# Performance work log

Hardware: AMD Instinct MI355X
Metric: run time of the kernel (lower is better)

The kernel has to match this reference:

```python
import jax, jax.numpy as jnp
import numpy as np

EPS = 1e-5
LAMB = 1.0
N_VARS = 40000
N_EDGES = 200000
N_CONF = 100000
FEAT = 128
DOM = 4
T_MAX = 3


def setup_inputs() -> dict:
    key = jax.random.key(0)
    ks = jax.random.split(key, 16)
    # initial node states: torch.rand then row-normalized (F.normalize dim=1)
    s = jax.random.uniform(ks[0], (N_VARS, FEAT), dtype=jnp.float32)
    state0 = s / jnp.maximum(jnp.linalg.norm(s, axis=1, keepdims=True), 1e-12)
    def lin(k, fan_in, shape):
        return jax.random.normal(k, shape, dtype=jnp.float32) / np.sqrt(fan_in)
    inp = {
        'state0': state0,
        'W1': lin(ks[1], 2 * FEAT, (2 * FEAT, FEAT)),
        'b1': jnp.zeros((FEAT,), jnp.float32),
        'W2': lin(ks[2], FEAT, (FEAT, FEAT)),
        'b2': jnp.zeros((FEAT,), jnp.float32),
        'ln_g': jnp.ones((FEAT,), jnp.float32),
        'ln_b': jnp.zeros((FEAT,), jnp.float32),
        'bn_g': jnp.ones((FEAT,), jnp.float32),
        'bn_b': jnp.zeros((FEAT,), jnp.float32),
        'Wd': lin(ks[3], FEAT, (FEAT, DOM)),
        'bd': jnp.zeros((DOM,), jnp.float32),
        # positive relation/confidence matrices so -log(...) is finite
        'relation': jax.random.uniform(ks[4], (DOM, DOM), jnp.float32, 0.1, 1.0),
        'confidence_mat': jax.random.uniform(ks[5], (DOM, DOM), jnp.float32, 0.1, 1.0),
        # positive degrees (divisor)
        'degrees': jax.random.uniform(ks[6], (N_VARS,), jnp.float32, 1.0, 33.0),
        'idx_left': jax.random.randint(ks[7], (N_EDGES,), 0, N_VARS, jnp.int32),
        'idx_right': jax.random.randint(ks[8], (N_EDGES,), 0, N_VARS, jnp.int32),
        'idx_left_pos': jax.random.randint(ks[9], (N_CONF,), 0, N_VARS, jnp.int32),
        'idx_right_pos': jax.random.randint(ks[10], (N_CONF,), 0, N_VARS, jnp.int32),
        'iterations': T_MAX,
    }
    return inp


def reference(state0, W1, b1, W2, b2, ln_g, ln_b, bn_g, bn_b, Wd, bd,
              relation, confidence_mat, degrees,
              idx_left, idx_right, idx_left_pos, idx_right_pos, iterations):
    N, F = state0.shape
    E = idx_left.shape[0]
    degs = degrees[:, None]

    def mlp(x):  # Linear-ReLU-Linear-ReLU-LayerNorm
        h = jax.nn.relu(x @ W1 + b1)
        h = jax.nn.relu(h @ W2 + b2)
        mu = jnp.mean(h, axis=-1, keepdims=True)
        var = jnp.var(h, axis=-1, keepdims=True)  # biased, like torch LayerNorm
        return ln_g * (h - mu) * jax.lax.rsqrt(var + EPS) + ln_b

    state = state0
    logits_list = []
    for _ in range(iterations):
        xl = state[idx_left]          # [E, F] gather
        xr = state[idx_right]
        # mpnn(in_right=xl, in_left=xr): in_lr = cat(xr, xl); in_rl = cat(xl, xr)
        msg = jnp.concatenate([jnp.concatenate([xr, xl], axis=1),
                               jnp.concatenate([xl, xr], axis=1)], axis=0)  # [2E, 2F]
        h = mlp(msg)
        agg = (jnp.zeros((N, F), state.dtype)
               .at[idx_left].add(h[:E])
               .at[idx_right].add(h[E:]))  # scatter-add messages
        rec = agg / degs
        # BatchNorm1d, training mode (batch stats over nodes)
        mu = jnp.mean(rec, axis=0)
        var = jnp.var(rec, axis=0)
        state = bn_g * (rec - mu) * jax.lax.rsqrt(var + EPS) + bn_b
        logits_list.append(state @ Wd + bd)

    phi = jax.nn.softmax(jnp.stack(logits_list, axis=1), axis=2)  # [N, T, D]
    T, D = phi.shape[1], phi.shape[2]
    all_phi = phi.reshape(N, T * D)

    def pair_loss(mat, il, ir, denom):
        pl = all_phi[il].reshape(-1, D)   # [E*T, D]
        pr = all_phi[ir].reshape(-1, D)
        s = jnp.sum((pl @ mat) * pr, axis=1)
        return jnp.sum(-jnp.log(s)) / denom

    n_conflicts = jnp.float32(E)
    n_confidence = jnp.float32(idx_left_pos.shape[0])
    loss = (pair_loss(relation, idx_left, idx_right, n_conflicts)
            + LAMB * pair_loss(confidence_mat, idx_left_pos, idx_right_pos, 10.0 * n_confidence))

    assignment = jnp.argmax(phi, axis=2).astype(jnp.int32)  # [N, T]
    valid = relation[assignment[idx_left], assignment[idx_right]]  # [E, T]
    edge_conflicts = 1.0 - valid
    n_conf = jnp.sum(edge_conflicts[:, -1])
    conflict_ratio = n_conf / n_conflicts
    return (loss, conflict_ratio, phi, edge_conflicts, assignment[:, -1], n_conf)
```

## Files before the change

kernel.cpp:

```cpp
#include <hip/hip_runtime.h>
#include <math.h>

#define N_VARS 40000
#define FEAT 128
#define N_EDGES 200000
#define N_MSG (2*N_EDGES)
#define N_CONFP 100000
#define T_ITERS 3
#define EPSF 1e-5f

#define NB_CONF 782
#define NB_LOSS 3517
#define NB_STAT 157
#define OUT_TOTAL 1120003
#define NCONF_SLOT 1120002

typedef short short8 __attribute__((ext_vector_type(8)));
typedef float floatx4 __attribute__((ext_vector_type(4)));
typedef unsigned short ushort4v __attribute__((ext_vector_type(4)));

__device__ __forceinline__ float scrub0(float x){
  unsigned u = __float_as_uint(x);
  return ((u & 0x7F800000u) == 0x7F800000u) ? 0.f : x;
}
__device__ __forceinline__ unsigned short f2bf_rne(float x){
  unsigned u = __float_as_uint(x);
  u += 0x7FFFu + ((u >> 16) & 1u);
  return (unsigned short)(u >> 16);
}
__device__ __forceinline__ float bf2f(unsigned short h){
  return __uint_as_float(((unsigned)h) << 16);
}
__device__ __forceinline__ unsigned cvtpk(float lo, float hi){
  unsigned r;
  asm("v_cvt_pk_bf16_f32 %0, %1, %2" : "=v"(r) : "v"(lo), "v"(hi));
  return r;
}

__global__ __launch_bounds__(256) void k_zero_int(int* __restrict__ p, int n){
  int i = blockIdx.x*256 + threadIdx.x;
  if (i < n) p[i] = 0;
}

__global__ __launch_bounds__(256) void k_hist(const int* __restrict__ idxL,
    const int* __restrict__ idxR, int* __restrict__ cnt){
  int m = blockIdx.x*256 + threadIdx.x;
  if (m < N_MSG){
    int t = (m < N_EDGES) ? idxL[m] : idxR[m - N_EDGES];
    atomicAdd(&cnt[t], 1);
  }
}
__global__ __launch_bounds__(256) void k_scan1(const int* __restrict__ cnt,
    int* __restrict__ pos, int* __restrict__ blk_tot){
  const int tid = threadIdx.x;
  const int idx = blockIdx.x*256 + tid;
  int v = (idx < N_VARS) ? cnt[idx] : 0;
  __shared__ int sh[256];
  sh[tid] = v;
  __syncthreads();
#pragma unroll
  for (int o = 1; o < 256; o <<= 1){
    int add = (tid >= o) ? sh[tid - o] : 0;
    __syncthreads();
    sh[tid] += add;
    __syncthreads();
  }
  if (idx < N_VARS) pos[idx] = sh[tid] - v;
  if (tid == 255) blk_tot[blockIdx.x] = sh[255];
}
__global__ __launch_bounds__(256) void k_scan2(const int* __restrict__ blk_tot,
    int* __restrict__ blk_off){
  const int tid = threadIdx.x;
  int v = (tid < NB_STAT) ? blk_tot[tid] : 0;
  __shared__ int sh[256];
  sh[tid] = v;
  __syncthreads();
#pragma unroll
  for (int o = 1; o < 256; o <<= 1){
    int add = (tid >= o) ? sh[tid - o] : 0;
    __syncthreads();
    sh[tid] += add;
    __syncthreads();
  }
  if (tid < NB_STAT) blk_off[tid] = sh[tid] - v;
}
__global__ __launch_bounds__(256) void k_scan3(int* __restrict__ pos,
    const int* __restrict__ blk_off){
  const int idx = blockIdx.x*256 + threadIdx.x;
  if (idx < N_VARS) pos[idx] += blk_off[blockIdx.x];
}
__global__ __launch_bounds__(256) void k_fill(const int* __restrict__ idxL,
    const int* __restrict__ idxR, int* __restrict__ pos,
    int* __restrict__ morder, int* __restrict__ nodeof){
  int m = blockIdx.x*256 + threadIdx.x;
  if (m < N_MSG){
    int t = (m < N_EDGES) ? idxL[m] : idxR[m - N_EDGES];
    int slot = atomicAdd(&pos[t], 1);
    morder[slot] = m;
    nodeof[slot] = t;
  }
}

__global__ __launch_bounds__(256) void k_prep(const float* __restrict__ W2,
                                              unsigned short* __restrict__ W2pack){
  int gid = blockIdx.x*256 + threadIdx.x;
  int lane = gid & 63;
  int ks = (gid >> 6) & 3;
  int ntg = gid >> 8;
  int kbase = ks*32 + (lane >> 4)*8;
  int n = ntg*16 + (lane & 15);
#pragma unroll
  for (int j = 0; j < 8; ++j)
    W2pack[gid*8 + j] = f2bf_rne(W2[(kbase + j)*FEAT + n]);
}
__global__ __launch_bounds__(256) void k_prep_w1(const float* __restrict__ W1,
                                                 unsigned short* __restrict__ W1pack){
  int gid = blockIdx.x*256 + threadIdx.x;
  int lane = gid & 63;
  int ks = (gid >> 6) & 3;
  int ntg = gid >> 8;
  int kbase = ks*32 + (lane >> 4)*8;
  int n = ntg*16 + (lane & 15);
#pragma unroll
  for (int j = 0; j < 8; ++j){
    int k = kbase + j;
    float v = (n < 128) ? W1[k*FEAT + n] : W1[(128 + k)*FEAT + (n - 128)];
    W1pack[gid*8 + j] = f2bf_rne(v);
  }
}

#define X_STRIDE 136
__global__ __launch_bounds__(256) void k_pq(const float* __restrict__ xf,
                                            const unsigned short* __restrict__ xb,
                                            int src_f32,
                                            const unsigned short* __restrict__ W1pack,
                                            const float* __restrict__ b1v,
                                            unsigned short* __restrict__ PQb,
                                            float* __restrict__ red,
                                            float4* __restrict__ recz){
  __shared__ __align__(16) unsigned short Xbf[32*X_STRIDE];
  const int tid = threadIdx.x;
  const int row0 = blockIdx.x * 32;
  if (blockIdx.x == 0) red[tid] = 0.f;
  {
    const int zid = blockIdx.x*256 + tid;
#pragma unroll
    for (int i = 0; i < 4; ++i)
      recz[zid + i*320000] = make_float4(0.f,0.f,0.f,0.f);
  }
  if (src_f32){
    const int c4 = (tid & 31)*4, g8 = tid >> 5;
#pragma unroll
    for (int r = 0; r < 4; ++r){
      int row = g8*4 + r;
      const float4 v = *(const float4*)&xf[(row0 + row)*FEAT + c4];
      uint2 uu;
      uu.x = cvtpk(v.x, v.y);
      uu.y = cvtpk(v.z, v.w);
      *(uint2*)&Xbf[row*X_STRIDE + c4] = uu;
    }
  } else {
    const int c8 = (tid & 15)*8, g16 = tid >> 4;
#pragma unroll
    for (int r = 0; r < 2; ++r){
      int row = r*16 + g16;
      *(short8*)&Xbf[row*X_STRIDE + c8] = *(const short8*)&xb[(row0 + row)*FEAT + c8];
    }
  }
  __syncthreads();
  const int w = tid >> 6, lane = tid & 63;
  const int quad = lane >> 4, mcol = lane & 15;
  float bi0 = 0.f, bi1 = 0.f, bi2 = 0.f, bi3 = 0.f;
  if (w >= 2){
    int nb = (w - 2)*64 + mcol;
    bi0 = b1v[nb]; bi1 = b1v[nb + 16]; bi2 = b1v[nb + 32]; bi3 = b1v[nb + 48];
  }
#pragma unroll
  for (int mt = 0; mt < 2; ++mt){
    floatx4 a0 = {bi0,bi0,bi0,bi0};
    floatx4 a1 = {bi1,bi1,bi1,bi1};
    floatx4 a2 = {bi2,bi2,bi2,bi2};
    floatx4 a3 = {bi3,bi3,bi3,bi3};
#pragma unroll
    for (int ks = 0; ks < 4; ++ks){
      short8 a = *(const short8*)&Xbf[(mt*16 + mcol)*X_STRIDE + ks*32 + quad*8];
      const unsigned short* bp = W1pack + ((w*16 + ks)*64 + lane)*8;
      short8 b0 = *(const short8*)(bp);
      short8 b1 = *(const short8*)(bp + 2048);
      short8 b2 = *(const short8*)(bp + 4096);
      short8 b3 = *(const short8*)(bp + 6144);
      a0 = __builtin_amdgcn_mfma_f32_16x16x32_bf16(a, b0, a0, 0, 0, 0);
      a1 = __builtin_amdgcn_mfma_f32_16x16x32_bf16(a, b1, a1, 0, 0, 0);
      a2 = __builtin_amdgcn_mfma_f32_16x16x32_bf16(a, b2, a2, 0, 0, 0);
      a3 = __builtin_amdgcn_mfma_f32_16x16x32_bf16(a, b3, a3, 0, 0, 0);
    }
#pragma unroll
    for (int reg = 0; reg < 4; ++reg){
      unsigned u01 = cvtpk(a0[reg], a1[reg]);
      unsigned u23 = cvtpk(a2[reg], a3[reg]);
      size_t base = (size_t)(row0 + mt*16 + quad*4 + reg)*(2*FEAT) + w*64 + mcol;
      PQb[base]      = (unsigned short)u01;
      PQb[base + 16] = (unsigned short)(u01 >> 16);
      PQb[base + 32] = (unsigned short)u23;
      PQb[base + 48] = (unsigned short)(u23 >> 16);
    }
  }
}

#define U_STRIDE 136
#define ZT_STRIDE 68

__global__ __launch_bounds__(256) void k_msgagg(const unsigned short* __restrict__ PQb,
    const unsigned short* __restrict__ W2pack,
    const float* __restrict__ b2v, const float* __restrict__ ln_g, const float* __restrict__ ln_b,
    const int* __restrict__ idxL, const int* __restrict__ idxR,
    const int* __restrict__ morder, const int* __restrict__ nodeof,
    const float* __restrict__ degrees,
    float* __restrict__ rec){
  __shared__ __align__(16) unsigned short Ubf[64*U_STRIDE];
  __shared__ int sTa[64], sTb[64];
  __shared__ float sDinv[64];
  __shared__ int sEdge[2];
  const int tid = threadIdx.x;
  const int s0 = blockIdx.x * 64;
  if (tid < 64){
    int m = morder[s0 + tid];
    int e = (m < N_EDGES) ? m : (m - N_EDGES);
    int l = idxL[e], r = idxR[e];
    int ta = (m < N_EDGES) ? l : r;
    sTa[tid] = ta;
    sTb[tid] = (m < N_EDGES) ? r : l;
    sDinv[tid] = 1.f / degrees[ta];
  } else if (tid == 64){
    sEdge[0] = (s0 == 0) ? -1 : nodeof[s0 - 1];
  } else if (tid == 65){
    sEdge[1] = (s0 + 64 >= N_MSG) ? -1 : nodeof[s0 + 64];
  }
  __syncthreads();
  {
    const int c8 = (tid & 15)*8, g16 = tid >> 4;
    short8 pb[4], qb[4];
#pragma unroll
    for (int r = 0; r < 4; ++r){
      int row = r*16 + g16;
      pb[r] = *(const short8*)&PQb[sTb[row]*(2*FEAT) + c8];
      qb[r] = *(const short8*)&PQb[sTa[row]*(2*FEAT) + FEAT + c8];
    }
#pragma unroll
    for (int r = 0; r < 4; ++r){
      int row = r*16 + g16;
      float f[8];
#pragma unroll
      for (int j = 0; j < 8; ++j)
        f[j] = fmaxf(bf2f((unsigned short)pb[r][j]) + bf2f((unsigned short)qb[r][j]), 0.f);
      uint4 uu;
      uu.x = cvtpk(f[0], f[1]);
      uu.y = cvtpk(f[2], f[3]);
      uu.z = cvtpk(f[4], f[5]);
      uu.w = cvtpk(f[6], f[7]);
      *(uint4*)&Ubf[row*U_STRIDE + c8] = uu;
    }
  }
  __syncthreads();
  const int w = tid >> 6, lane = tid & 63;
  const int quad = lane >> 4, mcol = lane & 15;
  const int rbase = w*16;
  floatx4 acc[8];
#pragma unroll
  for (int nt = 0; nt < 8; ++nt){
    float b = b2v[nt*16 + mcol];
    acc[nt] = (floatx4){b, b, b, b};
  }
#pragma unroll
  for (int ks = 0; ks < 4; ++ks){
    short8 a = *(const short8*)&Ubf[(rbase + mcol)*U_STRIDE + ks*32 + quad*8];
#pragma unroll
    for (int nt = 0; nt < 8; ++nt){
      short8 b = *(const short8*)(W2pack + ((nt*4 + ks)*64 + lane)*8);
      acc[nt] = __builtin_amdgcn_mfma_f32_16x16x32_bf16(a, b, acc[nt], 0, 0, 0);
    }
  }
  float z[8][4];
#pragma unroll
  for (int nt = 0; nt < 8; ++nt){
#pragma unroll
    for (int reg = 0; reg < 4; ++reg) z[nt][reg] = fmaxf(acc[nt][reg], 0.f);
  }
  float ps[4], pq[4];
#pragma unroll
  for (int reg = 0; reg < 4; ++reg){
    ps[reg] = 0.f; pq[reg] = 0.f;
#pragma unroll
    for (int nt = 0; nt < 8; ++nt){
      ps[reg] += z[nt][reg];
      pq[reg] += z[nt][reg]*z[nt][reg];
    }
  }
#pragma unroll
  for (int o = 1; o < 16; o <<= 1){
#pragma unroll
    for (int reg = 0; reg < 4; ++reg){
      ps[reg] += __shfl_xor(ps[reg], o);
      pq[reg] += __shfl_xor(pq[reg], o);
    }
  }
  float lgv[8], lbv[8];
#pragma unroll
  for (int nt = 0; nt < 8; ++nt){
    lgv[nt] = ln_g[nt*16 + mcol];
    lbv[nt] = ln_b[nt*16 + mcol];
  }
  unsigned obp[4][4];
#pragma unroll
  for (int reg = 0; reg < 4; ++reg){
    float mu = ps[reg] * (1.f/FEAT);
    float var = fmaxf(pq[reg] * (1.f/FEAT) - mu*mu, 0.f);
    float rv = rsqrtf(var + EPSF);
#pragma unroll
    for (int np = 0; np < 4; ++np){
      float o0 = scrub0(lgv[2*np  ]*(z[2*np  ][reg] - mu)*rv + lbv[2*np  ]);
      float o1 = scrub0(lgv[2*np+1]*(z[2*np+1][reg] - mu)*rv + lbv[2*np+1]);
      obp[reg][np] = cvtpk(o0, o1);
    }
  }
  __syncthreads();
#pragma unroll
  for (int reg = 0; reg < 4; ++reg){
    int row = rbase + quad*4 + reg;
#pragma unroll
    for (int np = 0; np < 4; ++np){
      unsigned u = obp[reg][np];
      Ubf[(2*np*16 + mcol)*ZT_STRIDE + row]       = (unsigned short)u;
      Ubf[((2*np+1)*16 + mcol)*ZT_STRIDE + row]   = (unsigned short)(u >> 16);
    }
  }
  __syncthreads();
  {
    const int col = tid & 127, h = tid >> 7;
    const int rbeg = h*32;
    ushort4v rv4[8];
#pragma unroll
    for (int k = 0; k < 8; ++k)
      rv4[k] = *(const ushort4v*)&Ubf[col*ZT_STRIDE + rbeg + k*4];
    float accv = 0.f;
    int cur = sTa[rbeg];
    bool part = (rbeg == 0) ? (sEdge[0] == cur) : (sTa[rbeg-1] == cur);
#pragma unroll
    for (int i = 0; i < 32; ++i){
      accv += bf2f((unsigned short)rv4[i >> 2][i & 3]);
      const int r = rbeg + i;
      int nxt = (r < 63) ? sTa[r + 1] : -2;
      const bool lastr = (i == 31);
      if (lastr | (nxt != cur)){
        bool tail = lastr && ((r == 63) ? (sEdge[1] == cur) : (nxt == cur));
        float v = accv * sDinv[r];
        float* dst = &rec[(size_t)cur*FEAT + col];
        if (part | tail) atomicAdd(dst, v);
        else *dst = v;
        accv = 0.f;
        cur = nxt;
        part = false;
      }
    }
  }
}

__global__ __launch_bounds__(256) void k_edge(const unsigned short* __restrict__ PQb,
    const unsigned short* __restrict__ W2pack,
    const float* __restrict__ b2v, const float* __restrict__ ln_g, const float* __restrict__ ln_b,
    const int* __restrict__ idxL, const int* __restrict__ idxR,
    float* __restrict__ agg){
  __shared__ __align__(16) unsigned short Ubf[32*U_STRIDE];
  __shared__ float sS[64], sQ[64];
  __shared__ int sTa[32], sTb[32];
  const int tid = threadIdx.x;
  const int m0 = blockIdx.x * 32;
  if (tid < 32){
    int m = m0 + tid;
    int e = (m < N_EDGES) ? m : (m - N_EDGES);
    int l = idxL[e], r = idxR[e];
    sTa[tid] = (m < N_EDGES) ? l : r;
    sTb[tid] = (m < N_EDGES) ? r : l;
  }
  __syncthreads();
  {
    const int c8 = (tid & 15)*8, g16 = tid >> 4;
#pragma unroll
    for (int r = 0; r < 2; ++r){
      int row = r*16 + g16;
      short8 pb = *(const short8*)&PQb[sTb[row]*(2*FEAT) + c8];
      short8 qb = *(const short8*)&PQb[sTa[row]*(2*FEAT) + FEAT + c8];
      float f[8];
#pragma unroll
      for (int j = 0; j < 8; ++j)
        f[j] = fmaxf(bf2f((unsigned short)pb[j]) + bf2f((unsigned short)qb[j]), 0.f);
      uint4 uu;
      uu.x = cvtpk(f[0], f[1]);
      uu.y = cvtpk(f[2], f[3]);
      uu.z = cvtpk(f[4], f[5]);
      uu.w = cvtpk(f[6], f[7]);
      *(uint4*)&Ubf[row*U_STRIDE + c8] = uu;
    }
  }
  __syncthreads();
  const int w = tid >> 6, lane = tid & 63;
  const int mt = w & 1, nhalf = w >> 1;
  const int quad = lane >> 4, mcol = lane & 15;
  float bb0 = b2v[nhalf*64 + 0*16 + mcol];
  float bb1 = b2v[nhalf*64 + 1*16 + mcol];
  float bb2 = b2v[nhalf*64 + 2*16 + mcol];
  float bb3 = b2v[nhalf*64 + 3*16 + mcol];
  floatx4 acc0 = {bb0,bb0,bb0,bb0};
  floatx4 acc1 = {bb1,bb1,bb1,bb1};
  floatx4 acc2 = {bb2,bb2,bb2,bb2};
  floatx4 acc3 = {bb3,bb3,bb3,bb3};
#pragma unroll
  for (int ks = 0; ks < 4; ++ks){
    short8 a = *(const short8*)&Ubf[(mt*16 + mcol)*U_STRIDE + ks*32 + quad*8];
    const unsigned short* bp = W2pack + ((nhalf*4*256) + ks*64 + lane)*8;
    short8 bq0 = *(const short8*)(bp);
    short8 bq1 = *(const short8*)(bp + 2048);
    short8 bq2 = *(const short8*)(bp + 4096);
    short8 bq3 = *(const short8*)(bp + 6144);
    acc0 = __builtin_amdgcn_mfma_f32_16x16x32_bf16(a, bq0, acc0, 0, 0, 0);
    acc1 = __builtin_amdgcn_mfma_f32_16x16x32_bf16(a, bq1, acc1, 0, 0, 0);
    acc2 = __builtin_amdgcn_mfma_f32_16x16x32_bf16(a, bq2, acc2, 0, 0, 0);
    acc3 = __builtin_amdgcn_mfma_f32_16x16x32_bf16(a, bq3, acc3, 0, 0, 0);
  }
  float z[4][4];
#pragma unroll
  for (int nt = 0; nt < 4; ++nt){
    floatx4 a4 = (nt == 0) ? acc0 : (nt == 1) ? acc1 : (nt == 2) ? acc2 : acc3;
#pragma unroll
    for (int reg = 0; reg < 4; ++reg) z[nt][reg] = fmaxf(a4[reg], 0.f);
  }
  float ps[4], pq[4];
#pragma unroll
  for (int reg = 0; reg < 4; ++reg){
    ps[reg] = z[0][reg] + z[1][reg] + z[2][reg] + z[3][reg];
    pq[reg] = z[0][reg]*z[0][reg] + z[1][reg]*z[1][reg] + z[2][reg]*z[2][reg] + z[3][reg]*z[3][reg];
  }
#pragma unroll
  for (int o = 1; o < 16; o <<= 1){
#pragma unroll
    for (int reg = 0; reg < 4; ++reg){
      ps[reg] += __shfl_xor(ps[reg], o);
      pq[reg] += __shfl_xor(pq[reg], o);
    }
  }
  if (mcol == 0){
#pragma unroll
    for (int reg = 0; reg < 4; ++reg){
      int row = mt*16 + quad*4 + reg;
      sS[nhalf*32 + row] = ps[reg];
      sQ[nhalf*32 + row] = pq[reg];
    }
  }
  __syncthreads();
  int colv[4]; float lgv[4], lbv[4];
#pragma unroll
  for (int nt = 0; nt < 4; ++nt){
    colv[nt] = nhalf*64 + nt*16 + mcol;
    lgv[nt] = ln_g[colv[nt]];
    lbv[nt] = ln_b[colv[nt]];
  }
#pragma unroll
  for (int reg = 0; reg < 4; ++reg){
    int row = mt*16 + quad*4 + reg;
    float s = sS[row] + sS[32 + row];
    float q = sQ[row] + sQ[32 + row];
    float mu = s * (1.f/FEAT);
    float var = fmaxf(q * (1.f/FEAT) - mu*mu, 0.f);
    float rv = rsqrtf(var + EPSF);
    int a = sTa[row];
#pragma unroll
    for (int nt = 0; nt < 4; ++nt){
      float o = scrub0(lgv[nt]*(z[nt][reg] - mu)*rv + lbv[nt]);
      atomicAdd(&agg[a*FEAT + colv[nt]], o);
    }
  }
}

__global__ __launch_bounds__(256) void k_stats(const float* __restrict__ src,
    const float* __restrict__ degrees, int divide, float* __restrict__ red){
  const int tid = threadIdx.x;
  const int j = tid & 127, half_sel = tid >> 7;
  const int n0 = blockIdx.x * 256;
  float s1 = 0.f, s2 = 0.f;
  for (int i = half_sel; i < 256; i += 2){
    int n = n0 + i;
    if (n < N_VARS){
      float v = src[n*FEAT + j];
      if (divide) v /= degrees[n];
      s1 += v;
      s2 += v*v;
    }
  }
  __shared__ float sh1[256], sh2[256];
  sh1[tid] = s1; sh2[tid] = s2;
  __syncthreads();
  if (half_sel == 0){
    atomicAdd(&red[j],       sh1[tid] + sh1[tid+128]);
    atomicAdd(&red[128 + j], sh2[tid] + sh2[tid+128]);
  }
}

__global__ __launch_bounds__(256) void k_bn(const float* __restrict__ src,
    const float* __restrict__ degrees, int divide, const float* __restrict__ red,
    const float* __restrict__ bn_g, const float* __restrict__ bn_b,
    const float* __restrict__ Wd, const float* __restrict__ bd,
    unsigned short* __restrict__ state_bf, int* __restrict__ asg,
    float* __restrict__ out_phi, float* __restrict__ out_asg, int t){
  const int w = threadIdx.x >> 6, l = threadIdx.x & 63;
  const int n = blockIdx.x*4 + w;
  const float invN = 1.f / (float)N_VARS;
  float mu0 = red[l]*invN,     mu1 = red[l+64]*invN;
  float v0  = fmaxf(red[128+l]*invN    - mu0*mu0, 0.f);
  float v1  = fmaxf(red[128+l+64]*invN - mu1*mu1, 0.f);
  float rv0 = rsqrtf(v0 + EPSF);
  float rv1 = rsqrtf(v1 + EPSF);
  float dinv = divide ? (1.f / degrees[n]) : 1.f;
  float r0 = src[n*FEAT + l]    * dinv;
  float r1 = src[n*FEAT + l+64] * dinv;
  float s0 = scrub0(bn_g[l]   *(r0 - mu0)*rv0 + bn_b[l]);
  float s1 = scrub0(bn_g[l+64]*(r1 - mu1)*rv1 + bn_b[l+64]);
  state_bf[n*FEAT + l]    = f2bf_rne(s0);
  state_bf[n*FEAT + l+64] = f2bf_rne(s1);
  float p[4];
#pragma unroll
  for (int d = 0; d < 4; ++d)
    p[d] = s0*Wd[l*4 + d] + s1*Wd[(l+64)*4 + d];
#pragma unroll
  for (int o = 32; o > 0; o >>= 1){
#pragma unroll
    for (int d = 0; d < 4; ++d) p[d] += __shfl_xor(p[d], o);
  }
  if (l == 0){
    float lg[4];
#pragma unroll
    for (int d = 0; d < 4; ++d) lg[d] = scrub0(p[d] + bd[d]);
    float mx = fmaxf(fmaxf(lg[0],lg[1]), fmaxf(lg[2],lg[3]));
    float ex[4]; float ssum = 0.f;
#pragma unroll
    for (int d = 0; d < 4; ++d){ ex[d] = expf(lg[d] - mx); ssum += ex[d]; }
    float inv = 1.f / ssum;
    int am = 0; float bv = -1.f;
#pragma unroll
    for (int d = 0; d < 4; ++d){
      float pv = scrub0(ex[d]*inv);
      out_phi[n*12 + t*4 + d] = pv;
      if (pv > bv){ bv = pv; am = d; }
    }
    asg[n*3 + t] = am;
    if (t == 2) out_asg[n] = (float)am;
  }
}

__global__ __launch_bounds__(256) void k_lossconf(const float* __restrict__ phi,
    const int* __restrict__ iL, const int* __restrict__ iR,
    const int* __restrict__ iLp, const int* __restrict__ iRp,
    const float* __restrict__ rel, const float* __restrict__ conf,
    const int* __restrict__ asg, float* __restrict__ out_ec,
    float* __restrict__ part_l1, float* __restrict__ part_l2,
    float* __restrict__ part_conf){
  if (blockIdx.x < NB_LOSS){
    const int m = blockIdx.x*256 + threadIdx.x;
    float p1 = 0.f, p2 = 0.f;
    if (m < N_EDGES*3){
      int e = m/3, tt = m - e*3;
      const float* pl = phi + iL[e]*12 + tt*4;
      const float* pr = phi + iR[e]*12 + tt*4;
      float s = 0.f;
#pragma unroll
      for (int j = 0; j < 4; ++j){
        float tj = 0.f;
#pragma unroll
        for (int i = 0; i < 4; ++i) tj += pl[i]*rel[i*4+j];
        s += tj*pr[j];
      }
      s = scrub0(s); s = fmaxf(s, 1e-35f);
      p1 = -logf(s);
    } else {
      int m2 = m - N_EDGES*3;
      if (m2 < N_CONFP*3){
        int e = m2/3, tt = m2 - e*3;
        const float* pl = phi + iLp[e]*12 + tt*4;
        const float* pr = phi + iRp[e]*12 + tt*4;
        float s = 0.f;
#pragma unroll
        for (int j = 0; j < 4; ++j){
          float tj = 0.f;
#pragma unroll
          for (int i = 0; i < 4; ++i) tj += pl[i]*conf[i*4+j];
          s += tj*pr[j];
        }
        s = scrub0(s); s = fmaxf(s, 1e-35f);
        p2 = -logf(s);
      }
    }
    __shared__ float sh1[256], sh2[256];
    sh1[threadIdx.x] = p1; sh2[threadIdx.x] = p2;
    __syncthreads();
    for (int k = 128; k > 0; k >>= 1){
      if (threadIdx.x < k){
        sh1[threadIdx.x] += sh1[threadIdx.x + k];
        sh2[threadIdx.x] += sh2[threadIdx.x + k];
      }
      __syncthreads();
    }
    if (threadIdx.x == 0){
      part_l1[blockIdx.x] = sh1[0];
      part_l2[blockIdx.x] = sh2[0];
    }
  } else {
    const int bid = blockIdx.x - NB_LOSS;
    const int e = bid*256 + threadIdx.x;
    float c2 = 0.f;
    if (e < N_EDGES){
      int l = iL[e], r = iR[e];
#pragma unroll
      for (int tt = 0; tt < 3; ++tt){
        int ai = asg[l*3+tt] & 3, bi = asg[r*3+tt] & 3;
        float c = scrub0(1.f - rel[ai*4 + bi]);
        out_ec[e*3 + tt] = c;
        if (tt == 2) c2 = c;
      }
    }
    __shared__ float sh[256];
    sh[threadIdx.x] = c2;
    __syncthreads();
    for (int k = 128; k > 0; k >>= 1){
      if (threadIdx.x < k) sh[threadIdx.x] += sh[threadIdx.x + k];
      __syncthreads();
    }
    if (threadIdx.x == 0) part_conf[bid] = sh[0];
  }
}

__global__ __launch_bounds__(256) void k_fin(const float* __restrict__ part_conf,
    const float* __restrict__ part_l1, const float* __restrict__ part_l2,
    float* __restrict__ out){
  const int tid = threadIdx.x;
  float a = 0.f, ca = 0.f, b = 0.f, cb = 0.f, c = 0.f;
  for (int i = tid; i < NB_LOSS; i += 256){
    float y = part_l1[i] - ca; float t = a + y; ca = (t - a) - y; a = t;
    float y2 = part_l2[i] - cb; float t2 = b + y2; cb = (t2 - b) - y2; b = t2;
  }
  for (int i = tid; i < NB_CONF; i += 256) c += part_conf[i];
  __shared__ float sh1[256], sh2[256], sh3[256];
  sh1[tid] = a; sh2[tid] = b; sh3[tid] = c;
  __syncthreads();
  for (int k = 128; k > 0; k >>= 1){
    if (tid < k){
      sh1[tid] += sh1[tid + k];
      sh2[tid] += sh2[tid + k];
      sh3[tid] += sh3[tid + k];
    }
    __syncthreads();
  }
  if (tid == 0){
    out[0] = sh1[0]/(float)N_EDGES + sh2[0]/(10.f*(float)N_CONFP);
    float nc = sh3[0];
    out[NCONF_SLOT] = nc;
    out[1] = nc / (float)N_EDGES;
  }
}

extern "C" void kernel_launch(void* const* d_in, const int* in_sizes, int n_in,
                              void* d_out, int out_size, void* d_ws, size_t ws_size,
                              hipStream_t stream){
  const float* state0  = (const float*)d_in[0];
  const float* W1      = (const float*)d_in[1];
  const float* b1v     = (const float*)d_in[2];
  const float* W2      = (const float*)d_in[3];
  const float* b2v     = (const float*)d_in[4];
  const float* ln_g    = (const float*)d_in[5];
  const float* ln_b    = (const float*)d_in[6];
  const float* bn_g    = (const float*)d_in[7];
  const float* bn_b    = (const float*)d_in[8];
  const float* Wd      = (const float*)d_in[9];
  const float* bd      = (const float*)d_in[10];
  const float* rel     = (const float*)d_in[11];
  const float* confm   = (const float*)d_in[12];
  const float* degrees = (const float*)d_in[13];
  const int* idxL = (const int*)d_in[14];
  const int* idxR = (const int*)d_in[15];
  const int* iLp  = (const int*)d_in[16];
  const int* iRp  = (const int*)d_in[17];

  char* ws = (char*)d_ws;
  unsigned short* state_bf = (unsigned short*)(ws);
  unsigned short* PQb  = (unsigned short*)(ws + 10240000);
  float*  recagg    = (float*)(ws + 30720000);
  int*    asg       = (int*)  (ws + 51200000);
  float*  red       = (float*)(ws + 51840768);
  float*  part_l1   = (float*)(ws + 51841792);
  float*  part_l2   = (float*)(ws + 51855860);
  float*  part_conf = (float*)(ws + 51869928);
  unsigned short* W2pack = (unsigned short*)(ws + 51873056);
  unsigned short* W1pack = (unsigned short*)(ws + 51905824);
  int*    pos       = (int*)(ws + 51971360);
  int*    cnt       = (int*)(ws + 52131360);
  int*    morder    = (int*)(ws + 52291360);
  int*    blk_tot   = (int*)(ws + 53891360);
  int*    blk_off   = (int*)(ws + 53892384);
  int*    nodeof    = (int*)(ws + 53893408);
  const int use_csr = (ws_size >= (size_t)55493408) ? 1 : 0;

  float* out     = (float*)d_out;
  float* out_phi = out + 2;
  float* out_ec  = out + 480002;
  float* out_asg = out + 1080002;

  k_prep<<<8, 256, 0, stream>>>(W2, W2pack);
  k_prep_w1<<<16, 256, 0, stream>>>(W1, W1pack);

  if (use_csr){
    k_zero_int<<<NB_STAT, 256, 0, stream>>>(cnt, N_VARS);
    k_hist<<<(N_MSG + 255)/256, 256, 0, stream>>>(idxL, idxR, cnt);
    k_scan1<<<NB_STAT, 256, 0, stream>>>(cnt, pos, blk_tot);
    k_scan2<<<1, 256, 0, stream>>>(blk_tot, blk_off);
    k_scan3<<<NB_STAT, 256, 0, stream>>>(pos, blk_off);
    k_fill<<<(N_MSG + 255)/256, 256, 0, stream>>>(idxL, idxR, pos, morder, nodeof);
  }

  for (int t = 0; t < T_ITERS; ++t){
    k_pq<<<N_VARS/32, 256, 0, stream>>>(state0, state_bf, (t == 0) ? 1 : 0, W1pack, b1v,
                                        PQb, red, (float4*)recagg);
    if (use_csr){
      k_msgagg<<<N_MSG/64, 256, 0, stream>>>(PQb, W2pack, b2v, ln_g, ln_b,
                                             idxL, idxR, morder, nodeof, degrees, recagg);
      k_stats<<<NB_STAT, 256, 0, stream>>>(recagg, degrees, 0, red);
      k_bn<<<N_VARS/4, 256, 0, stream>>>(recagg, degrees, 0, red, bn_g, bn_b, Wd, bd,
                                         state_bf, asg, out_phi, out_asg, t);
    } else {
      k_edge<<<N_MSG/32, 256, 0, stream>>>(PQb, W2pack, b2v, ln_g, ln_b, idxL, idxR, recagg);
      k_stats<<<NB_STAT, 256, 0, stream>>>(recagg, degrees, 1, red);
      k_bn<<<N_VARS/4, 256, 0, stream>>>(recagg, degrees, 1, red, bn_g, bn_b, Wd, bd,
                                         state_bf, asg, out_phi, out_asg, t);
    }
  }
  k_lossconf<<<NB_LOSS + NB_CONF, 256, 0, stream>>>(out_phi, idxL, idxR, iLp, iRp, rel, confm,
                                                    asg, out_ec, part_l1, part_l2, part_conf);
  k_fin<<<1, 256, 0, stream>>>(part_conf, part_l1, part_l2, out);
}
```

Before: 563.1 us.

## Merge weight prep kernels, widen stats grid, restructure loss and segment-break detection

Merges the two weight-packing kernels into one launch. Precomputes segment breaks in the message aggregation kernel with a wave ballot, and writes the transposed LayerNorm output as packed 64-bit stores instead of scalar 16-bit stores. Launches the column-statistics kernel with four times as many blocks, each covering 64 nodes. Restructures the pair loss so one thread handles all three iterations of an edge with vector loads and a fast log. These are several small independent tweaks, each aimed at launch overhead, LDS traffic or parallelism, at the cost of slightly less precise logs.

```diff
diff --git a/kernel.cpp b/kernel.cpp
--- a/kernel.cpp
+++ b/kernel.cpp
@@ -10,8 +10,9 @@
 #define EPSF 1e-5f
 
 #define NB_CONF 782
-#define NB_LOSS 3517
+#define NB_PAIR 1172
 #define NB_STAT 157
+#define NB_STAT2 625
 #define OUT_TOTAL 1120003
 #define NCONF_SLOT 1120002
 
@@ -101,31 +102,33 @@
   }
 }
 
-__global__ __launch_bounds__(256) void k_prep(const float* __restrict__ W2,
-                                              unsigned short* __restrict__ W2pack){
-  int gid = blockIdx.x*256 + threadIdx.x;
-  int lane = gid & 63;
-  int ks = (gid >> 6) & 3;
-  int ntg = gid >> 8;
-  int kbase = ks*32 + (lane >> 4)*8;
-  int n = ntg*16 + (lane & 15);
-#pragma unroll
-  for (int j = 0; j < 8; ++j)
-    W2pack[gid*8 + j] = f2bf_rne(W2[(kbase + j)*FEAT + n]);
-}
-__global__ __launch_bounds__(256) void k_prep_w1(const float* __restrict__ W1,
-                                                 unsigned short* __restrict__ W1pack){
-  int gid = blockIdx.x*256 + threadIdx.x;
-  int lane = gid & 63;
-  int ks = (gid >> 6) & 3;
-  int ntg = gid >> 8;
-  int kbase = ks*32 + (lane >> 4)*8;
-  int n = ntg*16 + (lane & 15);
-#pragma unroll
-  for (int j = 0; j < 8; ++j){
-    int k = kbase + j;
-    float v = (n < 128) ? W1[k*FEAT + n] : W1[(128 + k)*FEAT + (n - 128)];
-    W1pack[gid*8 + j] = f2bf_rne(v);
+__global__ __launch_bounds__(256) void k_prep2(const float* __restrict__ W2,
+                                               const float* __restrict__ W1,
+                                               unsigned short* __restrict__ W2pack,
+                                               unsigned short* __restrict__ W1pack){
+  if (blockIdx.x < 8){
+    int gid = blockIdx.x*256 + threadIdx.x;
+    int lane = gid & 63;
+    int ks = (gid >> 6) & 3;
+    int ntg = gid >> 8;
+    int kbase = ks*32 + (lane >> 4)*8;
+    int n = ntg*16 + (lane & 15);
+#pragma unroll
+    for (int j = 0; j < 8; ++j)
+      W2pack[gid*8 + j] = f2bf_rne(W2[(kbase + j)*FEAT + n]);
+  } else {
+    int gid = (blockIdx.x - 8)*256 + threadIdx.x;
+    int lane = gid & 63;
+    int ks = (gid >> 6) & 3;
+    int ntg = gid >> 8;
+    int kbase = ks*32 + (lane >> 4)*8;
+    int n = ntg*16 + (lane & 15);
+#pragma unroll
+    for (int j = 0; j < 8; ++j){
+      int k = kbase + j;
+      float v = (n < 128) ? W1[k*FEAT + n] : W1[(128 + k)*FEAT + (n - 128)];
+      W1pack[gid*8 + j] = f2bf_rne(v);
+    }
   }
 }
 
@@ -221,6 +224,7 @@
   __shared__ int sTa[64], sTb[64];
   __shared__ float sDinv[64];
   __shared__ int sEdge[2];
+  __shared__ unsigned sBrkLo, sBrkHi;
   const int tid = threadIdx.x;
   const int s0 = blockIdx.x * 64;
   if (tid < 64){
@@ -237,6 +241,11 @@
     sEdge[1] = (s0 + 64 >= N_MSG) ? -1 : nodeof[s0 + 64];
   }
   __syncthreads();
+  if (tid < 64){
+    bool d = (tid == 63) ? true : (sTa[tid + 1] != sTa[tid]);
+    unsigned long long b = __ballot(d ? 1 : 0);
+    if (tid == 0){ sBrkLo = (unsigned)b; sBrkHi = (unsigned)(b >> 32); }
+  }
   {
     const int c8 = (tid & 15)*8, g16 = tid >> 4;
     short8 pb[4], qb[4];
@@ -310,34 +319,35 @@
     lgv[nt] = ln_g[nt*16 + mcol];
     lbv[nt] = ln_b[nt*16 + mcol];
   }
-  unsigned obp[4][4];
+  float muv[4], rvv[4];
 #pragma unroll
   for (int reg = 0; reg < 4; ++reg){
     float mu = ps[reg] * (1.f/FEAT);
     float var = fmaxf(pq[reg] * (1.f/FEAT) - mu*mu, 0.f);
-    float rv = rsqrtf(var + EPSF);
-#pragma unroll
-    for (int np = 0; np < 4; ++np){
-      float o0 = scrub0(lgv[2*np  ]*(z[2*np  ][reg] - mu)*rv + lbv[2*np  ]);
-      float o1 = scrub0(lgv[2*np+1]*(z[2*np+1][reg] - mu)*rv + lbv[2*np+1]);
-      obp[reg][np] = cvtpk(o0, o1);
-    }
-  }
-  __syncthreads();
-#pragma unroll
-  for (int reg = 0; reg < 4; ++reg){
-    int row = rbase + quad*4 + reg;
-#pragma unroll
-    for (int np = 0; np < 4; ++np){
-      unsigned u = obp[reg][np];
-      Ubf[(2*np*16 + mcol)*ZT_STRIDE + row]       = (unsigned short)u;
-      Ubf[((2*np+1)*16 + mcol)*ZT_STRIDE + row]   = (unsigned short)(u >> 16);
-    }
+    muv[reg] = mu;
+    rvv[reg] = rsqrtf(var + EPSF);
+  }
+  unsigned w0p[8], w1p[8];
+#pragma unroll
+  for (int nt = 0; nt < 8; ++nt){
+    float o0 = scrub0(lgv[nt]*(z[nt][0] - muv[0])*rvv[0] + lbv[nt]);
+    float o1 = scrub0(lgv[nt]*(z[nt][1] - muv[1])*rvv[1] + lbv[nt]);
+    float o2 = scrub0(lgv[nt]*(z[nt][2] - muv[2])*rvv[2] + lbv[nt]);
+    float o3 = scrub0(lgv[nt]*(z[nt][3] - muv[3])*rvv[3] + lbv[nt]);
+    w0p[nt] = cvtpk(o0, o1);
+    w1p[nt] = cvtpk(o2, o3);
+  }
+  __syncthreads();
+#pragma unroll
+  for (int nt = 0; nt < 8; ++nt){
+    uint2 u; u.x = w0p[nt]; u.y = w1p[nt];
+    *(uint2*)&Ubf[(nt*16 + mcol)*ZT_STRIDE + rbase + quad*4] = u;
   }
   __syncthreads();
   {
     const int col = tid & 127, h = tid >> 7;
     const int rbeg = h*32;
+    const unsigned bm = __builtin_amdgcn_readfirstlane(h ? sBrkHi : sBrkLo);
     ushort4v rv4[8];
 #pragma unroll
     for (int k = 0; k < 8; ++k)
@@ -348,18 +358,17 @@
 #pragma unroll
     for (int i = 0; i < 32; ++i){
       accv += bf2f((unsigned short)rv4[i >> 2][i & 3]);
-      const int r = rbeg + i;
-      int nxt = (r < 63) ? sTa[r + 1] : -2;
-      const bool lastr = (i == 31);
-      if (lastr | (nxt != cur)){
-        bool tail = lastr && ((r == 63) ? (sEdge[1] == cur) : (nxt == cur));
+      const bool realbrk = (bm >> i) & 1u;
+      if ((i == 31) | realbrk){
+        const int r = rbeg + i;
+        bool cont = (i == 31) && ((r == 63) ? (sEdge[1] == cur) : !realbrk);
         float v = accv * sDinv[r];
         float* dst = &rec[(size_t)cur*FEAT + col];
-        if (part | tail) atomicAdd(dst, v);
+        if (part | cont) atomicAdd(dst, v);
         else *dst = v;
         accv = 0.f;
-        cur = nxt;
         part = false;
+        if (i < 31) cur = sTa[r + 1];
       }
     }
   }
@@ -485,16 +494,14 @@
     const float* __restrict__ degrees, int divide, float* __restrict__ red){
   const int tid = threadIdx.x;
   const int j = tid & 127, half_sel = tid >> 7;
-  const int n0 = blockIdx.x * 256;
+  const int n0 = blockIdx.x * 64;
   float s1 = 0.f, s2 = 0.f;
-  for (int i = half_sel; i < 256; i += 2){
+  for (int i = half_sel; i < 64; i += 2){
     int n = n0 + i;
-    if (n < N_VARS){
-      float v = src[n*FEAT + j];
-      if (divide) v /= degrees[n];
-      s1 += v;
-      s2 += v*v;
-    }
+    float v = src[n*FEAT + j];
+    if (divide) v /= degrees[n];
+    s1 += v;
+    s2 += v*v;
   }
   __shared__ float sh1[256], sh2[256];
   sh1[tid] = s1; sh2[tid] = s2;
@@ -563,40 +570,38 @@
     const int* __restrict__ asg, float* __restrict__ out_ec,
     float* __restrict__ part_l1, float* __restrict__ part_l2,
     float* __restrict__ part_conf){
-  if (blockIdx.x < NB_LOSS){
-    const int m = blockIdx.x*256 + threadIdx.x;
+  if (blockIdx.x < NB_PAIR){
+    const int e = blockIdx.x*256 + threadIdx.x;
     float p1 = 0.f, p2 = 0.f;
-    if (m < N_EDGES*3){
-      int e = m/3, tt = m - e*3;
-      const float* pl = phi + iL[e]*12 + tt*4;
-      const float* pr = phi + iR[e]*12 + tt*4;
-      float s = 0.f;
-#pragma unroll
-      for (int j = 0; j < 4; ++j){
-        float tj = 0.f;
-#pragma unroll
-        for (int i = 0; i < 4; ++i) tj += pl[i]*rel[i*4+j];
-        s += tj*pr[j];
+    if (e < N_EDGES + N_CONFP){
+      const int isrel = (e < N_EDGES);
+      const int l = isrel ? iL[e] : iLp[e - N_EDGES];
+      const int r = isrel ? iR[e] : iRp[e - N_EDGES];
+      const float* M = isrel ? rel : conf;
+      const float2* plp = (const float2*)(phi + (size_t)l*12);
+      const float2* prp = (const float2*)(phi + (size_t)r*12);
+      float L[12], R[12];
+#pragma unroll
+      for (int k = 0; k < 6; ++k){
+        float2 a = plp[k], b = prp[k];
+        L[2*k] = a.x; L[2*k+1] = a.y;
+        R[2*k] = b.x; R[2*k+1] = b.y;
       }
-      s = scrub0(s); s = fmaxf(s, 1e-35f);
-      p1 = -logf(s);
-    } else {
-      int m2 = m - N_EDGES*3;
-      if (m2 < N_CONFP*3){
-        int e = m2/3, tt = m2 - e*3;
-        const float* pl = phi + iLp[e]*12 + tt*4;
-        const float* pr = phi + iRp[e]*12 + tt*4;
+      float acc = 0.f;
+#pragma unroll
+      for (int tt = 0; tt < 3; ++tt){
+        const float* a = L + tt*4;
+        const float* b = R + tt*4;
         float s = 0.f;
 #pragma unroll
         for (int j = 0; j < 4; ++j){
-          float tj = 0.f;
-#pragma unroll
-          for (int i = 0; i < 4; ++i) tj += pl[i]*conf[i*4+j];
-          s += tj*pr[j];
+          float tj = a[0]*M[0*4+j] + a[1]*M[1*4+j] + a[2]*M[2*4+j] + a[3]*M[3*4+j];
+          s += tj*b[j];
         }
         s = scrub0(s); s = fmaxf(s, 1e-35f);
-        p2 = -logf(s);
+        acc -= __logf(s);
       }
+      if (isrel) p1 = acc; else p2 = acc;
     }
     __shared__ float sh1[256], sh2[256];
     sh1[threadIdx.x] = p1; sh2[threadIdx.x] = p2;
@@ -613,7 +618,7 @@
       part_l2[blockIdx.x] = sh2[0];
     }
   } else {
-    const int bid = blockIdx.x - NB_LOSS;
+    const int bid = blockIdx.x - NB_PAIR;
     const int e = bid*256 + threadIdx.x;
     float c2 = 0.f;
     if (e < N_EDGES){
@@ -642,7 +647,7 @@
     float* __restrict__ out){
   const int tid = threadIdx.x;
   float a = 0.f, ca = 0.f, b = 0.f, cb = 0.f, c = 0.f;
-  for (int i = tid; i < NB_LOSS; i += 256){
+  for (int i = tid; i < NB_PAIR; i += 256){
     float y = part_l1[i] - ca; float t = a + y; ca = (t - a) - y; a = t;
     float y2 = part_l2[i] - cb; float t2 = b + y2; cb = (t2 - b) - y2; b = t2;
   }
@@ -712,8 +717,7 @@
   float* out_ec  = out + 480002;
   float* out_asg = out + 1080002;
 
-  k_prep<<<8, 256, 0, stream>>>(W2, W2pack);
-  k_prep_w1<<<16, 256, 0, stream>>>(W1, W1pack);
+  k_prep2<<<24, 256, 0, stream>>>(W2, W1, W2pack, W1pack);
 
   if (use_csr){
     k_zero_int<<<NB_STAT, 256, 0, stream>>>(cnt, N_VARS);
@@ -730,17 +734,17 @@
     if (use_csr){
       k_msgagg<<<N_MSG/64, 256, 0, stream>>>(PQb, W2pack, b2v, ln_g, ln_b,
                                              idxL, idxR, morder, nodeof, degrees, recagg);
-      k_stats<<<NB_STAT, 256, 0, stream>>>(recagg, degrees, 0, red);
+      k_stats<<<NB_STAT2, 256, 0, stream>>>(recagg, degrees, 0, red);
       k_bn<<<N_VARS/4, 256, 0, stream>>>(recagg, degrees, 0, red, bn_g, bn_b, Wd, bd,
                                          state_bf, asg, out_phi, out_asg, t);
     } else {
       k_edge<<<N_MSG/32, 256, 0, stream>>>(PQb, W2pack, b2v, ln_g, ln_b, idxL, idxR, recagg);
-      k_stats<<<NB_STAT, 256, 0, stream>>>(recagg, degrees, 1, red);
+      k_stats<<<NB_STAT2, 256, 0, stream>>>(recagg, degrees, 1, red);
       k_bn<<<N_VARS/4, 256, 0, stream>>>(recagg, degrees, 1, red, bn_g, bn_b, Wd, bd,
                                          state_bf, asg, out_phi, out_asg, t);
     }
   }
-  k_lossconf<<<NB_LOSS + NB_CONF, 256, 0, stream>>>(out_phi, idxL, idxR, iLp, iRp, rel, confm,
+  k_lossconf<<<NB_PAIR + NB_CONF, 256, 0, stream>>>(out_phi, idxL, idxR, iLp, iRp, rel, confm,
                                                     asg, out_ec, part_l1, part_l2, part_conf);
   k_fin<<<1, 256, 0, stream>>>(part_conf, part_l1, part_l2, out);
 }
```

Measured after the change: 523.4 us. -7.0%, faster.
